# Kernel tuning notes

Measured on AMD Instinct MI355X. Metric: run time of the kernel, lower is better.

The kernel has to match this reference:

```python
import jax, jax.numpy as jnp
import numpy as np

D_MODEL, D_FF, N_EXPERTS, TOP_K = 1024, 4096, 8, 2
BATCH, SEQ = 4, 2048


def setup_inputs() -> dict:
    key = jax.random.key(0)
    ks = jax.random.split(key, 8)
    s_in = 1.0 / np.sqrt(D_MODEL)
    s_ff = 1.0 / np.sqrt(D_FF)
    return {
        "x": jax.random.normal(ks[0], (BATCH, SEQ, D_MODEL), dtype=jnp.float32),
        "W_gate": jax.random.uniform(ks[1], (D_MODEL, N_EXPERTS), jnp.float32, -s_in, s_in),
        "b_gate": jax.random.uniform(ks[2], (N_EXPERTS,), jnp.float32, -s_in, s_in),
        "W1": jax.random.uniform(ks[3], (N_EXPERTS, D_MODEL, D_FF), jnp.float32, -s_in, s_in),
        "b1": jax.random.uniform(ks[4], (N_EXPERTS, D_FF), jnp.float32, -s_in, s_in),
        "W2": jax.random.uniform(ks[5], (N_EXPERTS, D_FF, D_MODEL), jnp.float32, -s_ff, s_ff),
        "b2": jax.random.uniform(ks[6], (N_EXPERTS, D_MODEL), jnp.float32, -s_ff, s_ff),
    }


def reference(x, W_gate, b_gate, W1, b1, W2, b2):
    B, S, D = x.shape
    # Router
    logits = jnp.einsum("bsd,de->bse", x, W_gate) + b_gate           # [B,S,E]
    probs = jax.nn.softmax(logits, axis=-1)
    top_p, top_i = jax.lax.top_k(probs, TOP_K)                        # [B,S,k]
    top_p = top_p / jnp.sum(top_p, axis=-1, keepdims=True)
    
    x_flat = x.reshape(-1, D)                                         # [T,D]
    idx_flat = top_i.reshape(-1, TOP_K)                               # [T,k]
    p_flat = top_p.reshape(-1, TOP_K)                                 # [T,k]
    
    # Dense all-expert FFN (faithful to original: every expert on every token)
    h = jax.nn.relu(jnp.einsum("td,edf->etf", x_flat, W1) + b1[:, None, :])  # [E,T,F]
    expert_out = jnp.einsum("etf,efd->etd", h, W2) + b2[:, None, :]          # [E,T,D]
    expert_out = jnp.transpose(expert_out, (1, 0, 2))                 # [T,E,D]
    
    # Gather top-k expert outputs and combine
    sel = jnp.take_along_axis(expert_out, idx_flat[:, :, None], axis=1)  # [T,k,D]
    out_flat = jnp.sum(sel * p_flat[:, :, None], axis=1)              # [T,D]
    output = out_flat.reshape(B, S, D)
    
    # torch.var defaults to unbiased (ddof=1)
    load_balance_loss = jnp.var(jnp.mean(probs, axis=(0, 1)), ddof=1)
    return (output, load_balance_loss)
```

## Files before the change

kernel.cpp:

```cpp
#include <hip/hip_runtime.h>
#include <cstdint>
#include <cstddef>

#define D_MODEL 1024
#define D_FF    4096
#define NEXP    8
#define NTOK    8192
#define MAXT    136
#define CAP     (MAXT * 128)

typedef unsigned short ushort_t;
typedef __attribute__((ext_vector_type(8))) short   short8;
typedef __attribute__((ext_vector_type(4))) float   floatx4;
typedef __attribute__((ext_vector_type(4))) unsigned short ushort4v;

__device__ __forceinline__ ushort_t f2bf(float f) {
    union { float f; uint32_t u; } v; v.f = f;
    uint32_t r = v.u + 0x7fffu + ((v.u >> 16) & 1u);
    return (ushort_t)(r >> 16);
}

__device__ __forceinline__ floatx4 mfma16(short8 a, short8 b, floatx4 c) {
    return __builtin_amdgcn_mfma_f32_16x16x32_bf16(a, b, c, 0, 0, 0);
}

__device__ __forceinline__ void gload16(const ushort_t* g, ushort_t* l) {
    __builtin_amdgcn_global_load_lds(
        (const __attribute__((address_space(1))) void*)g,
        (__attribute__((address_space(3))) void*)l, 16, 0, 0);
}

__device__ __forceinline__ int tile_decode(const int* __restrict__ counts,
                                           int tm, int& e_out, int& row0) {
    int cnts[NEXP];
#pragma unroll
    for (int e = 0; e < NEXP; ++e) cnts[e] = counts[e];
    int b = 0, t = tm;
#pragma unroll
    for (int e = 0; e < NEXP; ++e) {
        int nt = (cnts[e] + 127) >> 7;
        if (t < nt) { e_out = e; row0 = b + t * 128; return 1; }
        t -= nt; b += nt * 128;
    }
    return 0;
}

__global__ __launch_bounds__(256)
void transpose_all(const float* __restrict__ W1, const float* __restrict__ W2,
                   ushort_t* __restrict__ W1T, ushort_t* __restrict__ W2T)
{
    __shared__ float t[64][65];
    int bid = blockIdx.x;
    const float* in; ushort_t* out; int R, C, rt, ct;
    if (bid < 8192) {
        int e = bid >> 10, rem = bid & 1023;
        R = D_MODEL; C = D_FF; rt = rem >> 6; ct = rem & 63;
        in = W1 + (size_t)e * R * C; out = W1T + (size_t)e * R * C;
    } else {
        int e = (bid - 8192) >> 10, rem = bid & 1023;
        R = D_FF; C = D_MODEL; rt = rem >> 4; ct = rem & 15;
        in = W2 + (size_t)e * R * C; out = W2T + (size_t)e * R * C;
    }
    int r0 = rt * 64, c0 = ct * 64, tid = threadIdx.x;
    int lr = tid >> 4, lc4 = (tid & 15) * 4;
#pragma unroll
    for (int p = 0; p < 4; ++p) {
        int rr = p * 16 + lr;
        float4 v = *(const float4*)(in + (size_t)(r0 + rr) * C + c0 + lc4);
        t[rr][lc4] = v.x; t[rr][lc4 + 1] = v.y; t[rr][lc4 + 2] = v.z; t[rr][lc4 + 3] = v.w;
    }
    __syncthreads();
    int orw = tid >> 3, j0 = (tid & 7) * 8;
#pragma unroll
    for (int p = 0; p < 2; ++p) {
        int orow = p * 32 + orw;
        ushort_t pk[8];
#pragma unroll
        for (int i = 0; i < 8; ++i) pk[i] = f2bf(t[j0 + i][orow]);
        *(short8*)(out + (size_t)(c0 + orow) * R + r0 + j0) = *(short8*)pk;
    }
}

__global__ __launch_bounds__(256)
void router_kernel(const float* __restrict__ x, const float* __restrict__ Wg,
                   const float* __restrict__ bg,
                   int* __restrict__ counts, int* __restrict__ slot_tok,
                   float* __restrict__ slot_p, float* __restrict__ psum)
{
    __shared__ float bsum[NEXP];
    int tid = threadIdx.x;
    if (tid < NEXP) bsum[tid] = 0.f;
    __syncthreads();

    int t = (blockIdx.x * 256 + tid) >> 6;
    int l = tid & 63;
    const float* xr = x + (size_t)t * D_MODEL;
    float acc[NEXP] = {0.f,0.f,0.f,0.f,0.f,0.f,0.f,0.f};
#pragma unroll 4
    for (int c = 0; c < D_MODEL / 64; ++c) {
        int d = c * 64 + l;
        float xv = xr[d];
        const float4* wr = (const float4*)(Wg + (size_t)d * NEXP);
        float4 w0 = wr[0], w1 = wr[1];
        acc[0] += xv * w0.x; acc[1] += xv * w0.y;
        acc[2] += xv * w0.z; acc[3] += xv * w0.w;
        acc[4] += xv * w1.x; acc[5] += xv * w1.y;
        acc[6] += xv * w1.z; acc[7] += xv * w1.w;
    }
#pragma unroll
    for (int off = 32; off >= 1; off >>= 1)
#pragma unroll
        for (int e = 0; e < NEXP; ++e)
            acc[e] += __shfl_xor(acc[e], off);

    if (l == 0) {
        float lg[NEXP], mx = -1e30f;
#pragma unroll
        for (int e = 0; e < NEXP; ++e) { lg[e] = acc[e] + bg[e]; mx = fmaxf(mx, lg[e]); }
        float pr[NEXP], s = 0.f;
#pragma unroll
        for (int e = 0; e < NEXP; ++e) { pr[e] = __expf(lg[e] - mx); s += pr[e]; }
        float inv = 1.f / s;
#pragma unroll
        for (int e = 0; e < NEXP; ++e) pr[e] *= inv;
        int e0 = 0;
#pragma unroll
        for (int e = 1; e < NEXP; ++e) if (pr[e] > pr[e0]) e0 = e;
        int e1 = (e0 == 0) ? 1 : 0;
#pragma unroll
        for (int e = 0; e < NEXP; ++e) if (e != e0 && pr[e] > pr[e1]) e1 = e;
        float pnorm = 1.f / (pr[e0] + pr[e1]);
        int s0 = atomicAdd(&counts[e0], 1);
        slot_tok[e0 * NTOK + s0] = t; slot_p[e0 * NTOK + s0] = pr[e0] * pnorm;
        int s1 = atomicAdd(&counts[e1], 1);
        slot_tok[e1 * NTOK + s1] = t; slot_p[e1 * NTOK + s1] = pr[e1] * pnorm;
#pragma unroll
        for (int e = 0; e < NEXP; ++e) atomicAdd(&bsum[e], pr[e]);
    }
    __syncthreads();
    if (tid < NEXP) atomicAdd(&psum[tid], bsum[tid]);
}

__global__ __launch_bounds__(256)
void gather_kernel(const float* __restrict__ x, const int* __restrict__ counts,
                   const int* __restrict__ slot_tok, const float* __restrict__ slot_p,
                   ushort_t* __restrict__ xg, float* __restrict__ tok_prob,
                   int* __restrict__ tcount, int* __restrict__ tok2row)
{
    __shared__ int sb[NEXP + 1];
    int row = blockIdx.x, tid = threadIdx.x;
    if (tid == 0) {
        int b = 0;
#pragma unroll
        for (int e = 0; e < NEXP; ++e) { sb[e] = b; b += ((counts[e] + 127) >> 7) << 7; }
        sb[NEXP] = b;
    }
    __syncthreads();
    if (row >= sb[NEXP]) return;
    int e = 0;
    while (e < NEXP - 1 && row >= sb[e + 1]) ++e;
    int lr = row - sb[e];
    int tok = -1; float pr = 0.f;
    if (lr < counts[e]) { tok = slot_tok[e * NTOK + lr]; pr = slot_p[e * NTOK + lr]; }
    if (tid == 0) {
        tok_prob[row] = pr;
        if (tok >= 0) {
            int s = atomicAdd(&tcount[tok], 1);
            tok2row[tok * 2 + s] = row;
        }
    }
    ushort_t* dst = xg + (size_t)row * D_MODEL;
    if (tok >= 0) {
        float4 v = ((const float4*)(x + (size_t)tok * D_MODEL))[tid];
        ushort4v o; o.x = f2bf(v.x); o.y = f2bf(v.y); o.z = f2bf(v.z); o.w = f2bf(v.w);
        *(ushort4v*)(dst + tid * 4) = o;
    } else {
        *(ushort4v*)(dst + tid * 4) = ushort4v{0, 0, 0, 0};
    }
}

template <int EPI>
__global__ __launch_bounds__(256, 2)
void gemm_tile(const ushort_t* __restrict__ A, const ushort_t* __restrict__ B,
               int K, int N, const int* __restrict__ counts,
               int row_lo, int row_hi,
               ushort_t* __restrict__ Hout, const float* __restrict__ bias,
               float* __restrict__ Yout)
{
    int NX = gridDim.x;
    int nwg = NX * (int)gridDim.y;
    int lin0 = blockIdx.y * NX + blockIdx.x;
    int cpx = nwg >> 3;
    int lin = (lin0 & 7) * cpx + (lin0 >> 3);
    int sid = lin >> 4, wi = lin & 15;
    int nsx = NX >> 2;
    int sx = sid % nsx, sy = sid / nsx;
    int colbase = ((sx << 2) + (wi & 3)) * 128;
    int tm = (sy << 2) + (wi >> 2);

    int e, row0;
    if (!tile_decode(counts, tm, e, row0)) return;
    if (row0 < row_lo || row0 >= row_hi) return;

    __shared__ ushort_t smem[128 * 64 * 2];
    ushort_t* As = smem;
    ushort_t* Bs = smem + 128 * 64;

    int tid = threadIdx.x;
    int w = tid >> 6, l = tid & 63;
    int q = l >> 4, ml = l & 15;
    int wm = w >> 1, wn = w & 1;

    const ushort_t* Ab = A + (size_t)row0 * K;
    const ushort_t* Bb = B + ((size_t)e * N + colbase) * K;

    const ushort_t* ag[4]; const ushort_t* bg[4];
    ushort_t* al[4]; ushort_t* bl[4];
#pragma unroll
    for (int i = 0; i < 4; ++i) {
        int rr = (i * 4 + w) * 8 + (l >> 3);
        int cc = ((l & 7) ^ (rr & 7)) * 8;
        ag[i] = Ab + (size_t)rr * K + cc;
        bg[i] = Bb + (size_t)rr * K + cc;
        al[i] = As + (i * 4 + w) * 512;
        bl[i] = Bs + (i * 4 + w) * 512;
    }

    floatx4 acc[4][4];
#pragma unroll
    for (int i = 0; i < 4; ++i)
#pragma unroll
        for (int j = 0; j < 4; ++j) acc[i][j] = floatx4{0.f, 0.f, 0.f, 0.f};

    int nst = K >> 6;
    for (int s = 0; s < nst; ++s) {
#pragma unroll
        for (int i = 0; i < 4; ++i) {
            gload16(ag[i], al[i]);
            gload16(bg[i], bl[i]);
            ag[i] += 64; bg[i] += 64;
        }
        __syncthreads();
#pragma unroll
        for (int kk = 0; kk < 2; ++kk) {
            int cb = kk * 4 + q;
            short8 av[4], bv[4];
#pragma unroll
            for (int mi = 0; mi < 4; ++mi) {
                int m = wm * 64 + mi * 16 + ml;
                av[mi] = *(const short8*)(As + m * 64 + ((cb ^ (m & 7)) * 8));
            }
#pragma unroll
            for (int ni = 0; ni < 4; ++ni) {
                int n = wn * 64 + ni * 16 + ml;
                bv[ni] = *(const short8*)(Bs + n * 64 + ((cb ^ (n & 7)) * 8));
            }
#pragma unroll
            for (int mi = 0; mi < 4; ++mi)
#pragma unroll
                for (int ni = 0; ni < 4; ++ni)
                    acc[mi][ni] = mfma16(av[mi], bv[ni], acc[mi][ni]);
        }
        __syncthreads();
    }

    float bv4[4];
#pragma unroll
    for (int ni = 0; ni < 4; ++ni)
        bv4[ni] = bias[e * N + colbase + wn * 64 + ni * 16 + ml];

    if (EPI == 0) {
        ushort_t* ct = smem;
#pragma unroll
        for (int mi = 0; mi < 4; ++mi)
#pragma unroll
            for (int ni = 0; ni < 4; ++ni)
#pragma unroll
                for (int r = 0; r < 4; ++r) {
                    float v = acc[mi][ni][r] + bv4[ni];
                    v = v > 0.f ? v : 0.f;
                    ct[(wm * 64 + mi * 16 + q * 4 + r) * 128 + wn * 64 + ni * 16 + ml] = f2bf(v);
                }
        __syncthreads();
#pragma unroll
        for (int i = 0; i < 8; ++i) {
            int idx = tid + i * 256;
            int r = idx >> 4, c8 = idx & 15;
            *(short8*)(Hout + (size_t)(row0 + r) * D_FF + colbase + c8 * 8) =
                *(const short8*)(ct + r * 128 + c8 * 8);
        }
    } else {
#pragma unroll
        for (int mi = 0; mi < 4; ++mi)
#pragma unroll
            for (int ni = 0; ni < 4; ++ni)
#pragma unroll
                for (int r = 0; r < 4; ++r) {
                    int row = row0 + wm * 64 + mi * 16 + q * 4 + r;
                    int col = colbase + wn * 64 + ni * 16 + ml;
                    Yout[(size_t)row * N + col] = acc[mi][ni][r] + bv4[ni];
                }
    }
}

__global__ __launch_bounds__(256)
void combine_kernel(const float* __restrict__ y, const int* __restrict__ tok2row,
                    const float* __restrict__ tok_prob, float* __restrict__ out,
                    const float* __restrict__ psum, float* __restrict__ loss_out)
{
    int t = blockIdx.x;
    if (t == 0 && threadIdx.x == 0) {
        float me[NEXP], m = 0.f;
#pragma unroll
        for (int e = 0; e < NEXP; ++e) { me[e] = psum[e] * (1.f / NTOK); m += me[e] * (1.f / NEXP); }
        float v = 0.f;
#pragma unroll
        for (int e = 0; e < NEXP; ++e) v += (me[e] - m) * (me[e] - m);
        loss_out[0] = v * (1.f / (NEXP - 1));
    }
    int r0 = tok2row[t * 2], r1 = tok2row[t * 2 + 1];
    float p0 = tok_prob[r0], p1 = tok_prob[r1];
    int c = threadIdx.x;
    float4 a = ((const float4*)(y + (size_t)r0 * D_MODEL))[c];
    float4 b = ((const float4*)(y + (size_t)r1 * D_MODEL))[c];
    float4 o;
    o.x = p0 * a.x + p1 * b.x;
    o.y = p0 * a.y + p1 * b.y;
    o.z = p0 * a.z + p1 * b.z;
    o.w = p0 * a.w + p1 * b.w;
    ((float4*)(out + (size_t)t * D_MODEL))[c] = o;
}

extern "C" void kernel_launch(void* const* d_in, const int* in_sizes, int n_in,
                              void* d_out, int out_size, void* d_ws, size_t ws_size,
                              hipStream_t stream)
{
    const float* x  = (const float*)d_in[0];
    const float* Wg = (const float*)d_in[1];
    const float* bg = (const float*)d_in[2];
    const float* W1 = (const float*)d_in[3];
    const float* b1 = (const float*)d_in[4];
    const float* W2 = (const float*)d_in[5];
    const float* b2 = (const float*)d_in[6];
    float* out = (float*)d_out;

    char* ws = (char*)d_ws;
    size_t off = 0;
    auto alloc = [&](size_t bytes) -> char* {
        char* p = ws + off;
        off = (off + bytes + 255) & ~(size_t)255;
        return p;
    };
    int*      counts   = (int*)alloc(NEXP * 4);
    float*    psum     = (float*)alloc(NEXP * 4);
    int*      tcount   = (int*)alloc(NTOK * 4);
    size_t zero_bytes = off;
    float*    tok_prob = (float*)alloc(CAP * 4);
    int*      tok2row  = (int*)alloc((size_t)NTOK * 2 * 4);
    int*      slot_tok = (int*)alloc((size_t)NEXP * NTOK * 4);
    float*    slot_p   = (float*)alloc((size_t)NEXP * NTOK * 4);
    ushort_t* xg       = (ushort_t*)alloc((size_t)CAP * D_MODEL * 2);
    ushort_t* W1T      = (ushort_t*)alloc((size_t)NEXP * D_MODEL * D_FF * 2);
    ushort_t* W2T      = (ushort_t*)alloc((size_t)NEXP * D_MODEL * D_FF * 2);
    float*    ybuf     = (float*)alloc((size_t)CAP * D_MODEL * 4);
    size_t fixed = off;
    size_t h_full = (size_t)CAP * D_FF * 2;

    int NC = 1;
    if (ws_size < fixed + h_full) NC = 4;
    if (NC == 4 && ws_size < fixed + h_full / 4) NC = 16;
    if (ws_size < fixed + h_full / NC) return;
    int chunk_rows = CAP / NC;
    ushort_t* hbuf = (ushort_t*)alloc(h_full / NC);

    hipMemsetAsync(d_ws, 0, zero_bytes, stream);

    transpose_all<<<16384, 256, 0, stream>>>(W1, W2, W1T, W2T);
    router_kernel<<<NTOK / 4, 256, 0, stream>>>(x, Wg, bg, counts, slot_tok, slot_p, psum);
    gather_kernel<<<CAP, 256, 0, stream>>>(x, counts, slot_tok, slot_p, xg,
                                           tok_prob, tcount, tok2row);
    for (int c = 0; c < NC; ++c) {
        int lo = c * chunk_rows, hi = lo + chunk_rows;
        ushort_t* h_eff = hbuf - (ptrdiff_t)lo * D_FF;
        gemm_tile<0><<<dim3(D_FF / 128, MAXT), 256, 0, stream>>>(
            xg, W1T, D_MODEL, D_FF, counts, lo, hi, h_eff, b1, nullptr);
        gemm_tile<1><<<dim3(D_MODEL / 128, MAXT), 256, 0, stream>>>(
            h_eff, W2T, D_FF, D_MODEL, counts, lo, hi, nullptr, b2, ybuf);
    }
    combine_kernel<<<NTOK, 256, 0, stream>>>(ybuf, tok2row, tok_prob, out, psum,
                                             out + (size_t)out_size - 1);
    (void)in_sizes; (void)n_in;
}
```

Measured before the change: 881.0 us.

## Double-buffer LDS tiles in expert GEMM to overlap global loads with MFMA

Doubles the shared-memory buffer and prefetches the next K-stage's A/B tiles into the alternate buffer, using explicit vmcnt waits so compute on the current stage overlaps in-flight global-to-LDS loads. Replaces __syncthreads with raw s_barrier plus a scheduling barrier. The cost is twice the LDS per workgroup (64KB), which may reduce occupancy. Correctness relies on the direct-to-LDS loads being tracked by vmcnt and on the count of 8 outstanding ops per stage.

```diff
diff --git a/kernel.cpp b/kernel.cpp
--- a/kernel.cpp
+++ b/kernel.cpp
@@ -202,9 +202,7 @@
     if (!tile_decode(counts, tm, e, row0)) return;
     if (row0 < row_lo || row0 >= row_hi) return;
 
-    __shared__ ushort_t smem[128 * 64 * 2];
-    ushort_t* As = smem;
-    ushort_t* Bs = smem + 128 * 64;
+    __shared__ ushort_t smem[128 * 64 * 2 * 2];
 
     int tid = threadIdx.x;
     int w = tid >> 6, l = tid & 63;
@@ -215,16 +213,26 @@
     const ushort_t* Bb = B + ((size_t)e * N + colbase) * K;
 
     const ushort_t* ag[4]; const ushort_t* bg[4];
-    ushort_t* al[4]; ushort_t* bl[4];
+    int lofs[4];
 #pragma unroll
     for (int i = 0; i < 4; ++i) {
         int rr = (i * 4 + w) * 8 + (l >> 3);
         int cc = ((l & 7) ^ (rr & 7)) * 8;
         ag[i] = Ab + (size_t)rr * K + cc;
         bg[i] = Bb + (size_t)rr * K + cc;
-        al[i] = As + (i * 4 + w) * 512;
-        bl[i] = Bs + (i * 4 + w) * 512;
-    }
+        lofs[i] = (i * 4 + w) * 512;
+    }
+
+#define STAGE(p)                                                           \
+    do {                                                                   \
+        ushort_t* base_ = smem + (p) * 16384;                              \
+        _Pragma("unroll")                                                  \
+        for (int i_ = 0; i_ < 4; ++i_) {                                   \
+            gload16(ag[i_], base_ + lofs[i_]);                             \
+            gload16(bg[i_], base_ + 8192 + lofs[i_]);                      \
+            ag[i_] += 64; bg[i_] += 64;                                    \
+        }                                                                  \
+    } while (0)
 
     floatx4 acc[4][4];
 #pragma unroll
@@ -233,14 +241,19 @@
         for (int j = 0; j < 4; ++j) acc[i][j] = floatx4{0.f, 0.f, 0.f, 0.f};
 
     int nst = K >> 6;
+    STAGE(0);
     for (int s = 0; s < nst; ++s) {
-#pragma unroll
-        for (int i = 0; i < 4; ++i) {
-            gload16(ag[i], al[i]);
-            gload16(bg[i], bl[i]);
-            ag[i] += 64; bg[i] += 64;
+        int p = s & 1;
+        if (s + 1 < nst) {
+            STAGE(p ^ 1);
+            asm volatile("s_waitcnt vmcnt(8)" ::: "memory");
+        } else {
+            asm volatile("s_waitcnt vmcnt(0)" ::: "memory");
         }
-        __syncthreads();
+        __builtin_amdgcn_s_barrier();
+        __builtin_amdgcn_sched_barrier(0);
+        const ushort_t* As = smem + p * 16384;
+        const ushort_t* Bs = As + 8192;
 #pragma unroll
         for (int kk = 0; kk < 2; ++kk) {
             int cb = kk * 4 + q;
@@ -261,8 +274,9 @@
                 for (int ni = 0; ni < 4; ++ni)
                     acc[mi][ni] = mfma16(av[mi], bv[ni], acc[mi][ni]);
         }
-        __syncthreads();
-    }
+        __builtin_amdgcn_s_barrier();
+    }
+#undef STAGE
 
     float bv4[4];
 #pragma unroll
```

Measured after the change: 879.8 us. About the same (-0.1%).
